# Kernel tuning notes

Measured on AMD Instinct MI355X. Metric: run time of the kernel, lower is better.

The kernel has to match this reference:

```python
import jax, jax.numpy as jnp
import numpy as np

EPS = 1e-7  # tf.keras.backend.epsilon()
ROUTING = 3
C, L = 32, 32

def squash(s):
    # 'Dynamic routing between capsules' squash: (|s|^2/(1+|s|^2)) * s/|s|
    n = jnp.linalg.norm(s, axis=-1, keepdims=True)
    return (n ** 2 / (1 + n ** 2) / (n + EPS)) * s

def setup_inputs() -> dict:
    key = jax.random.key(0)
    k1, k2 = jax.random.split(key)
    B, H, Wd, iC, iL = 32, 8, 8, 32, 32
    inputs = jax.random.normal(k1, (B, H, Wd, iC, iL), dtype=jnp.float32)
    N = H * Wd * iC  # 2048 input capsules
    # glorot_uniform for W: [N, input_L, C*L]
    limit = float(np.sqrt(6.0 / (iL + C * L)))
    W = jax.random.uniform(k2, (N, iL, C * L), minval=-limit, maxval=limit, dtype=jnp.float32)
    biases = jnp.zeros((C, L), dtype=jnp.float32)  # 'zeros' initializer
    return {"inputs": inputs, "W": W, "biases": biases}

def reference(inputs, W, biases):
    B = inputs.shape[0]
    N, iL = W.shape[0], W.shape[1]
    x = inputs.reshape(B, N, iL)
    # per-capsule prediction: u[b,j,k] = sum_i x[b,j,i] * W[j,i,k]
    u = jnp.einsum('bji,jik->bjk', x, W).reshape(B, N, C, L)
    b = jnp.zeros((B, N, C, 1), dtype=u.dtype)
    v = jnp.zeros((B, C, L), dtype=u.dtype)
    for r in range(ROUTING):
        c = jax.nn.softmax(b, axis=2)                 # coupling coeffs over C
        s = jnp.sum(u * c, axis=1) + biases           # [B,C,L]
        # NOTE: CapsuleAttentionBlock applied here in original (source not
        # provided in this module); treated as identity.
        v = squash(s)                                 # [B,C,L]
        if r < ROUTING - 1:
            b = b + jnp.sum(u * v[:, None, :, :], axis=-1, keepdims=True)
    return v
```

## Files before the change

kernel.cpp:

```cpp
#include <hip/hip_runtime.h>
#include <hip/hip_bf16.h>

#define NB    32
#define NCAP  2048
#define CDIM  32
#define LDIM  32
#define ILEN  32
#define CL    1024

__device__ inline unsigned short f32_to_bf16_rne(float f) {
    unsigned int u = __float_as_uint(f);
    unsigned int r = 0x7FFFu + ((u >> 16) & 1u);
    u += r;
    return (unsigned short)(u >> 16);
}
__device__ inline float bf16_to_f32(unsigned short h) {
    return __uint_as_float(((unsigned int)h) << 16);
}

__global__ __launch_bounds__(256) void compute_u(const float* __restrict__ x,
                                                 const float* __restrict__ W,
                                                 unsigned short* __restrict__ u) {
    const int j  = blockIdx.x >> 2;
    const int kq = blockIdx.x & 3;
    const int t  = threadIdx.x;

    __shared__ float wl[32 * 256];
    __shared__ float xs[32 * 32];

    const float* Wj = W + (size_t)j * (ILEN * CL) + kq * 256;
#pragma unroll
    for (int it = 0; it < 8; ++it) {
        int f   = t + it * 256;
        int i   = f >> 6;
        int col = (f & 63) << 2;
        float4 v = *(const float4*)(Wj + (size_t)i * CL + col);
        *(float4*)(wl + i * 256 + col) = v;
    }
    {
        int b = t >> 3;
        int i = (t & 7) << 2;
        float4 v = *(const float4*)(x + (size_t)b * (NCAP * ILEN) + (size_t)j * ILEN + i);
        *(float4*)(xs + b * 32 + i) = v;
    }
    __syncthreads();

    const int lane = t & 63;
    const int wv   = t >> 6;

    float4 acc[8];
#pragma unroll
    for (int bb = 0; bb < 8; ++bb) acc[bb] = make_float4(0.f, 0.f, 0.f, 0.f);

#pragma unroll 4
    for (int i = 0; i < 32; ++i) {
        float4 w4 = *(const float4*)(wl + i * 256 + (lane << 2));
#pragma unroll
        for (int bb = 0; bb < 8; ++bb) {
            float xv = xs[(wv * 8 + bb) * 32 + i];
            acc[bb].x += xv * w4.x;
            acc[bb].y += xv * w4.y;
            acc[bb].z += xv * w4.z;
            acc[bb].w += xv * w4.w;
        }
    }

    const int k = kq * 256 + (lane << 2);
#pragma unroll
    for (int bb = 0; bb < 8; ++bb) {
        int b = wv * 8 + bb;
        ushort4 o;
        o.x = f32_to_bf16_rne(acc[bb].x);
        o.y = f32_to_bf16_rne(acc[bb].y);
        o.z = f32_to_bf16_rne(acc[bb].z);
        o.w = f32_to_bf16_rne(acc[bb].w);
        *(ushort4*)(u + ((size_t)b * NCAP + j) * CL + k) = o;
    }
}

__global__ __launch_bounds__(256) void route_pass(const unsigned short* __restrict__ u,
                                                  const float* __restrict__ vlog,
                                                  float* __restrict__ s_out) {
    const int b  = blockIdx.x;
    const int jc = blockIdx.y;
    const int t  = threadIdx.x;

    __shared__ float vl[1024];
    __shared__ float blog[32];
    __shared__ float cpl[32];

    {
        float4 v = *(const float4*)(vlog + b * 1024 + t * 4);
        *(float4*)(vl + t * 4) = v;
    }
    __syncthreads();

    const int c  = t >> 3;
    const int l4 = (t & 7) << 2;
    const float4 vme = *(const float4*)(vl + c * 32 + l4);

    float4 acc = make_float4(0.f, 0.f, 0.f, 0.f);
    const unsigned short* ub = u + ((size_t)b * NCAP + (size_t)jc * 64) * CL + t * 4;

    ushort4 uu = *(const ushort4*)(ub);
    for (int jj = 0; jj < 64; ++jj) {
        float4 uf;
        uf.x = bf16_to_f32(uu.x);
        uf.y = bf16_to_f32(uu.y);
        uf.z = bf16_to_f32(uu.z);
        uf.w = bf16_to_f32(uu.w);

        ushort4 uu_next;
        if (jj + 1 < 64) uu_next = *(const ushort4*)(ub + (size_t)(jj + 1) * CL);

        float p = uf.x * vme.x + uf.y * vme.y + uf.z * vme.z + uf.w * vme.w;
        p += __shfl_xor(p, 1, 64);
        p += __shfl_xor(p, 2, 64);
        p += __shfl_xor(p, 4, 64);
        if ((t & 7) == 0) blog[c] = p;
        __syncthreads();

        if (t < 64) {
            int ci = t & 31;
            float val = blog[ci];
            float m = val;
            m = fmaxf(m, __shfl_xor(m, 16, 64));
            m = fmaxf(m, __shfl_xor(m, 8, 64));
            m = fmaxf(m, __shfl_xor(m, 4, 64));
            m = fmaxf(m, __shfl_xor(m, 2, 64));
            m = fmaxf(m, __shfl_xor(m, 1, 64));
            float e = __expf(val - m);
            float ssum = e;
            ssum += __shfl_xor(ssum, 16, 64);
            ssum += __shfl_xor(ssum, 8, 64);
            ssum += __shfl_xor(ssum, 4, 64);
            ssum += __shfl_xor(ssum, 2, 64);
            ssum += __shfl_xor(ssum, 1, 64);
            if (t < 32) cpl[ci] = e / ssum;
        }
        __syncthreads();

        float cw = cpl[c];
        acc.x += cw * uf.x;
        acc.y += cw * uf.y;
        acc.z += cw * uf.z;
        acc.w += cw * uf.w;
        uu = uu_next;
    }

    float* sp = s_out + b * 1024 + c * 32 + l4;
    atomicAdd(sp + 0, acc.x);
    atomicAdd(sp + 1, acc.y);
    atomicAdd(sp + 2, acc.z);
    atomicAdd(sp + 3, acc.w);
}

__global__ __launch_bounds__(256) void squash_kernel(const float* __restrict__ s,
                                                     const float* __restrict__ biases,
                                                     float* __restrict__ vout,
                                                     float* __restrict__ vlog_out,
                                                     const float* __restrict__ vprev) {
    const int b = blockIdx.x;
    const int t = threadIdx.x;

    float4 sv = *(const float4*)(s + b * 1024 + t * 4);
    float4 bi = *(const float4*)(biases + t * 4);
    sv.x += bi.x; sv.y += bi.y; sv.z += bi.z; sv.w += bi.w;

    float n2 = sv.x * sv.x + sv.y * sv.y + sv.z * sv.z + sv.w * sv.w;
    n2 += __shfl_xor(n2, 1, 64);
    n2 += __shfl_xor(n2, 2, 64);
    n2 += __shfl_xor(n2, 4, 64);

    float n = sqrtf(n2);
    float f = n2 / (1.f + n2) / (n + 1e-7f);

    float4 v;
    v.x = f * sv.x; v.y = f * sv.y; v.z = f * sv.z; v.w = f * sv.w;
    *(float4*)(vout + b * 1024 + t * 4) = v;

    if (vlog_out != nullptr) {
        float4 a = make_float4(0.f, 0.f, 0.f, 0.f);
        if (vprev != nullptr) a = *(const float4*)(vprev + b * 1024 + t * 4);
        float4 o;
        o.x = v.x + a.x; o.y = v.y + a.y; o.z = v.z + a.z; o.w = v.w + a.w;
        *(float4*)(vlog_out + b * 1024 + t * 4) = o;
    }
}

extern "C" void kernel_launch(void* const* d_in, const int* in_sizes, int n_in,
                              void* d_out, int out_size, void* d_ws, size_t ws_size,
                              hipStream_t stream) {
    const float* x      = (const float*)d_in[0];
    const float* W      = (const float*)d_in[1];
    const float* biases = (const float*)d_in[2];
    float* out = (float*)d_out;

    unsigned short* u = (unsigned short*)d_ws;
    float* fb = (float*)((char*)d_ws + (size_t)NB * NCAP * CL * 2);
    float* s0   = fb + 0 * 32768;
    float* s1   = fb + 1 * 32768;
    float* s2   = fb + 2 * 32768;
    float* zv   = fb + 3 * 32768;
    float* v0   = fb + 4 * 32768;
    float* vl2  = fb + 5 * 32768;
    float* vdmp = fb + 6 * 32768;

    hipMemsetAsync(fb, 0, 4 * 32768 * sizeof(float), stream);

    compute_u<<<NCAP * 4, 256, 0, stream>>>(x, W, u);

    dim3 rg(NB, 32);
    route_pass<<<rg, 256, 0, stream>>>(u, zv, s0);
    squash_kernel<<<NB, 256, 0, stream>>>(s0, biases, v0, nullptr, nullptr);
    route_pass<<<rg, 256, 0, stream>>>(u, v0, s1);
    squash_kernel<<<NB, 256, 0, stream>>>(s1, biases, vdmp, vl2, v0);
    route_pass<<<rg, 256, 0, stream>>>(u, vl2, s2);
    squash_kernel<<<NB, 256, 0, stream>>>(s2, biases, out, nullptr, nullptr);
}
```

Before: 556.6 us.

## Restructure routing pass to per-wave softmax without block barriers and partial sums

The routing kernel is rewritten so each wavefront processes whole input capsules independently. It computes the 32 agreement logits and their softmax with in-wave shuffles, removing the two __syncthreads per capsule and 16-byte bf16 loads. Partial sums are reduced in LDS and written to per-chunk buffers that squash sums, which replaces the atomics and the memset. The first pass skips the softmax and uses a uniform 1/32 coefficient, and compute_u now stores x transposed in LDS to allow vector loads.

```diff
diff --git a/kernel.cpp b/kernel.cpp
--- a/kernel.cpp
+++ b/kernel.cpp
@@ -3,19 +3,24 @@
 
 #define NB    32
 #define NCAP  2048
-#define CDIM  32
-#define LDIM  32
+#define CL    1024
 #define ILEN  32
-#define CL    1024
 
 __device__ inline unsigned short f32_to_bf16_rne(float f) {
     unsigned int u = __float_as_uint(f);
-    unsigned int r = 0x7FFFu + ((u >> 16) & 1u);
-    u += r;
+    u += 0x7FFFu + ((u >> 16) & 1u);
     return (unsigned short)(u >> 16);
 }
-__device__ inline float bf16_to_f32(unsigned short h) {
-    return __uint_as_float(((unsigned int)h) << 16);
+
+__device__ inline void unpack8(uint4 a, float* f) {
+    f[0] = __uint_as_float(a.x << 16);
+    f[1] = __uint_as_float(a.x & 0xFFFF0000u);
+    f[2] = __uint_as_float(a.y << 16);
+    f[3] = __uint_as_float(a.y & 0xFFFF0000u);
+    f[4] = __uint_as_float(a.z << 16);
+    f[5] = __uint_as_float(a.z & 0xFFFF0000u);
+    f[6] = __uint_as_float(a.w << 16);
+    f[7] = __uint_as_float(a.w & 0xFFFF0000u);
 }
 
 __global__ __launch_bounds__(256) void compute_u(const float* __restrict__ x,
@@ -34,34 +39,40 @@
         int f   = t + it * 256;
         int i   = f >> 6;
         int col = (f & 63) << 2;
-        float4 v = *(const float4*)(Wj + (size_t)i * CL + col);
-        *(float4*)(wl + i * 256 + col) = v;
+        *(float4*)(wl + i * 256 + col) = *(const float4*)(Wj + (size_t)i * CL + col);
     }
     {
-        int b = t >> 3;
-        int i = (t & 7) << 2;
-        float4 v = *(const float4*)(x + (size_t)b * (NCAP * ILEN) + (size_t)j * ILEN + i);
-        *(float4*)(xs + b * 32 + i) = v;
+        int b  = t >> 3;
+        int i4 = (t & 7) << 2;
+        float4 v = *(const float4*)(x + ((size_t)b * NCAP + j) * ILEN + i4);
+        xs[(i4 + 0) * 32 + b] = v.x;
+        xs[(i4 + 1) * 32 + b] = v.y;
+        xs[(i4 + 2) * 32 + b] = v.z;
+        xs[(i4 + 3) * 32 + b] = v.w;
     }
     __syncthreads();
 
     const int lane = t & 63;
     const int wv   = t >> 6;
 
-    float4 acc[8];
-#pragma unroll
-    for (int bb = 0; bb < 8; ++bb) acc[bb] = make_float4(0.f, 0.f, 0.f, 0.f);
+    float acc[8][4];
+#pragma unroll
+    for (int bb = 0; bb < 8; ++bb)
+#pragma unroll
+        for (int q = 0; q < 4; ++q) acc[bb][q] = 0.f;
 
 #pragma unroll 4
     for (int i = 0; i < 32; ++i) {
         float4 w4 = *(const float4*)(wl + i * 256 + (lane << 2));
+        float4 xa = *(const float4*)(xs + i * 32 + wv * 8);
+        float4 xb = *(const float4*)(xs + i * 32 + wv * 8 + 4);
+        float xv[8] = {xa.x, xa.y, xa.z, xa.w, xb.x, xb.y, xb.z, xb.w};
 #pragma unroll
         for (int bb = 0; bb < 8; ++bb) {
-            float xv = xs[(wv * 8 + bb) * 32 + i];
-            acc[bb].x += xv * w4.x;
-            acc[bb].y += xv * w4.y;
-            acc[bb].z += xv * w4.z;
-            acc[bb].w += xv * w4.w;
+            acc[bb][0] += xv[bb] * w4.x;
+            acc[bb][1] += xv[bb] * w4.y;
+            acc[bb][2] += xv[bb] * w4.z;
+            acc[bb][3] += xv[bb] * w4.w;
         }
     }
 
@@ -70,92 +81,112 @@
     for (int bb = 0; bb < 8; ++bb) {
         int b = wv * 8 + bb;
         ushort4 o;
-        o.x = f32_to_bf16_rne(acc[bb].x);
-        o.y = f32_to_bf16_rne(acc[bb].y);
-        o.z = f32_to_bf16_rne(acc[bb].z);
-        o.w = f32_to_bf16_rne(acc[bb].w);
+        o.x = f32_to_bf16_rne(acc[bb][0]);
+        o.y = f32_to_bf16_rne(acc[bb][1]);
+        o.z = f32_to_bf16_rne(acc[bb][2]);
+        o.w = f32_to_bf16_rne(acc[bb][3]);
         *(ushort4*)(u + ((size_t)b * NCAP + j) * CL + k) = o;
     }
 }
 
+template<bool HAS_V>
 __global__ __launch_bounds__(256) void route_pass(const unsigned short* __restrict__ u,
                                                   const float* __restrict__ vlog,
-                                                  float* __restrict__ s_out) {
-    const int b  = blockIdx.x;
-    const int jc = blockIdx.y;
-    const int t  = threadIdx.x;
-
-    __shared__ float vl[1024];
-    __shared__ float blog[32];
-    __shared__ float cpl[32];
-
-    {
-        float4 v = *(const float4*)(vlog + b * 1024 + t * 4);
-        *(float4*)(vl + t * 4) = v;
-    }
+                                                  float* __restrict__ spart) {
+    const int b    = blockIdx.x;
+    const int jc   = blockIdx.y;
+    const int t    = threadIdx.x;
+    const int wv   = t >> 6;
+    const int lane = t & 63;
+    const int c0   = lane >> 2;
+    const int sub  = lane & 3;
+    const int e0   = c0 * 32 + sub * 8;
+
+    float vme0[8], vme1[8];
+    if (HAS_V) {
+        const float* vb = vlog + b * CL;
+        *(float4*)(vme0)     = *(const float4*)(vb + e0);
+        *(float4*)(vme0 + 4) = *(const float4*)(vb + e0 + 4);
+        *(float4*)(vme1)     = *(const float4*)(vb + e0 + 512);
+        *(float4*)(vme1 + 4) = *(const float4*)(vb + e0 + 516);
+    }
+
+    const int jbase = jc * 128 + wv * 32;
+    const unsigned short* ub = u + ((size_t)b * NCAP + jbase) * CL;
+
+    float acc0[8], acc1[8];
+#pragma unroll
+    for (int e = 0; e < 8; ++e) { acc0[e] = 0.f; acc1[e] = 0.f; }
+
+    uint4 a0 = *(const uint4*)(ub + 0 * CL + e0);
+    uint4 g0 = *(const uint4*)(ub + 0 * CL + e0 + 512);
+    uint4 a1 = *(const uint4*)(ub + 1 * CL + e0);
+    uint4 g1 = *(const uint4*)(ub + 1 * CL + e0 + 512);
+
+    for (int jj = 0; jj < 32; ++jj) {
+        int jn = (jj + 2 < 32) ? (jj + 2) : 31;
+        uint4 a2 = *(const uint4*)(ub + (size_t)jn * CL + e0);
+        uint4 g2 = *(const uint4*)(ub + (size_t)jn * CL + e0 + 512);
+
+        float uf0[8], uf1[8];
+        unpack8(a0, uf0);
+        unpack8(g0, uf1);
+
+        float cw0, cw1;
+        if (HAS_V) {
+            float p0 = 0.f, p1 = 0.f;
+#pragma unroll
+            for (int e = 0; e < 8; ++e) { p0 += uf0[e] * vme0[e]; p1 += uf1[e] * vme1[e]; }
+            p0 += __shfl_xor(p0, 1); p0 += __shfl_xor(p0, 2);
+            p1 += __shfl_xor(p1, 1); p1 += __shfl_xor(p1, 2);
+            float m = fmaxf(p0, p1);
+            m = fmaxf(m, __shfl_xor(m, 4));
+            m = fmaxf(m, __shfl_xor(m, 8));
+            m = fmaxf(m, __shfl_xor(m, 16));
+            m = fmaxf(m, __shfl_xor(m, 32));
+            float ex0 = __expf(p0 - m);
+            float ex1 = __expf(p1 - m);
+            float ssum = ex0 + ex1;
+            ssum += __shfl_xor(ssum, 4);
+            ssum += __shfl_xor(ssum, 8);
+            ssum += __shfl_xor(ssum, 16);
+            ssum += __shfl_xor(ssum, 32);
+            float inv = __builtin_amdgcn_rcpf(ssum);
+            cw0 = ex0 * inv;
+            cw1 = ex1 * inv;
+        } else {
+            cw0 = 0.03125f;
+            cw1 = 0.03125f;
+        }
+#pragma unroll
+        for (int e = 0; e < 8; ++e) {
+            acc0[e] += cw0 * uf0[e];
+            acc1[e] += cw1 * uf1[e];
+        }
+        a0 = a1; g0 = g1; a1 = a2; g1 = g2;
+    }
+
+    __shared__ float red[4][1024];
+    *(float4*)(&red[wv][e0])       = *(float4*)(acc0);
+    *(float4*)(&red[wv][e0 + 4])   = *(float4*)(acc0 + 4);
+    *(float4*)(&red[wv][e0 + 512]) = *(float4*)(acc1);
+    *(float4*)(&red[wv][e0 + 516]) = *(float4*)(acc1 + 4);
     __syncthreads();
 
-    const int c  = t >> 3;
-    const int l4 = (t & 7) << 2;
-    const float4 vme = *(const float4*)(vl + c * 32 + l4);
-
-    float4 acc = make_float4(0.f, 0.f, 0.f, 0.f);
-    const unsigned short* ub = u + ((size_t)b * NCAP + (size_t)jc * 64) * CL + t * 4;
-
-    ushort4 uu = *(const ushort4*)(ub);
-    for (int jj = 0; jj < 64; ++jj) {
-        float4 uf;
-        uf.x = bf16_to_f32(uu.x);
-        uf.y = bf16_to_f32(uu.y);
-        uf.z = bf16_to_f32(uu.z);
-        uf.w = bf16_to_f32(uu.w);
-
-        ushort4 uu_next;
-        if (jj + 1 < 64) uu_next = *(const ushort4*)(ub + (size_t)(jj + 1) * CL);
-
-        float p = uf.x * vme.x + uf.y * vme.y + uf.z * vme.z + uf.w * vme.w;
-        p += __shfl_xor(p, 1, 64);
-        p += __shfl_xor(p, 2, 64);
-        p += __shfl_xor(p, 4, 64);
-        if ((t & 7) == 0) blog[c] = p;
-        __syncthreads();
-
-        if (t < 64) {
-            int ci = t & 31;
-            float val = blog[ci];
-            float m = val;
-            m = fmaxf(m, __shfl_xor(m, 16, 64));
-            m = fmaxf(m, __shfl_xor(m, 8, 64));
-            m = fmaxf(m, __shfl_xor(m, 4, 64));
-            m = fmaxf(m, __shfl_xor(m, 2, 64));
-            m = fmaxf(m, __shfl_xor(m, 1, 64));
-            float e = __expf(val - m);
-            float ssum = e;
-            ssum += __shfl_xor(ssum, 16, 64);
-            ssum += __shfl_xor(ssum, 8, 64);
-            ssum += __shfl_xor(ssum, 4, 64);
-            ssum += __shfl_xor(ssum, 2, 64);
-            ssum += __shfl_xor(ssum, 1, 64);
-            if (t < 32) cpl[ci] = e / ssum;
-        }
-        __syncthreads();
-
-        float cw = cpl[c];
-        acc.x += cw * uf.x;
-        acc.y += cw * uf.y;
-        acc.z += cw * uf.z;
-        acc.w += cw * uf.w;
-        uu = uu_next;
-    }
-
-    float* sp = s_out + b * 1024 + c * 32 + l4;
-    atomicAdd(sp + 0, acc.x);
-    atomicAdd(sp + 1, acc.y);
-    atomicAdd(sp + 2, acc.z);
-    atomicAdd(sp + 3, acc.w);
-}
-
-__global__ __launch_bounds__(256) void squash_kernel(const float* __restrict__ s,
+    const int o = t * 4;
+    float4 r0 = *(float4*)(&red[0][o]);
+    float4 r1 = *(float4*)(&red[1][o]);
+    float4 r2 = *(float4*)(&red[2][o]);
+    float4 r3 = *(float4*)(&red[3][o]);
+    float4 r;
+    r.x = (r0.x + r1.x) + (r2.x + r3.x);
+    r.y = (r0.y + r1.y) + (r2.y + r3.y);
+    r.z = (r0.z + r1.z) + (r2.z + r3.z);
+    r.w = (r0.w + r1.w) + (r2.w + r3.w);
+    *(float4*)(spart + ((size_t)b * 16 + jc) * CL + o) = r;
+}
+
+__global__ __launch_bounds__(256) void squash_kernel(const float* __restrict__ spart,
                                                      const float* __restrict__ biases,
                                                      float* __restrict__ vout,
                                                      float* __restrict__ vlog_out,
@@ -163,28 +194,33 @@
     const int b = blockIdx.x;
     const int t = threadIdx.x;
 
-    float4 sv = *(const float4*)(s + b * 1024 + t * 4);
+    float4 sv = make_float4(0.f, 0.f, 0.f, 0.f);
+#pragma unroll
+    for (int p = 0; p < 16; ++p) {
+        float4 q = *(const float4*)(spart + ((size_t)b * 16 + p) * CL + t * 4);
+        sv.x += q.x; sv.y += q.y; sv.z += q.z; sv.w += q.w;
+    }
     float4 bi = *(const float4*)(biases + t * 4);
     sv.x += bi.x; sv.y += bi.y; sv.z += bi.z; sv.w += bi.w;
 
     float n2 = sv.x * sv.x + sv.y * sv.y + sv.z * sv.z + sv.w * sv.w;
-    n2 += __shfl_xor(n2, 1, 64);
-    n2 += __shfl_xor(n2, 2, 64);
-    n2 += __shfl_xor(n2, 4, 64);
+    n2 += __shfl_xor(n2, 1);
+    n2 += __shfl_xor(n2, 2);
+    n2 += __shfl_xor(n2, 4);
 
     float n = sqrtf(n2);
-    float f = n2 / (1.f + n2) / (n + 1e-7f);
+    float f = n2 / ((1.f + n2) * (n + 1e-7f));
 
     float4 v;
     v.x = f * sv.x; v.y = f * sv.y; v.z = f * sv.z; v.w = f * sv.w;
-    *(float4*)(vout + b * 1024 + t * 4) = v;
+    *(float4*)(vout + b * CL + t * 4) = v;
 
     if (vlog_out != nullptr) {
         float4 a = make_float4(0.f, 0.f, 0.f, 0.f);
-        if (vprev != nullptr) a = *(const float4*)(vprev + b * 1024 + t * 4);
+        if (vprev != nullptr) a = *(const float4*)(vprev + b * CL + t * 4);
         float4 o;
         o.x = v.x + a.x; o.y = v.y + a.y; o.z = v.z + a.z; o.w = v.w + a.w;
-        *(float4*)(vlog_out + b * 1024 + t * 4) = o;
+        *(float4*)(vlog_out + b * CL + t * 4) = o;
     }
 }
 
@@ -197,24 +233,19 @@
     float* out = (float*)d_out;
 
     unsigned short* u = (unsigned short*)d_ws;
-    float* fb = (float*)((char*)d_ws + (size_t)NB * NCAP * CL * 2);
-    float* s0   = fb + 0 * 32768;
-    float* s1   = fb + 1 * 32768;
-    float* s2   = fb + 2 * 32768;
-    float* zv   = fb + 3 * 32768;
-    float* v0   = fb + 4 * 32768;
-    float* vl2  = fb + 5 * 32768;
-    float* vdmp = fb + 6 * 32768;
-
-    hipMemsetAsync(fb, 0, 4 * 32768 * sizeof(float), stream);
+    float* fb    = (float*)((char*)d_ws + (size_t)NB * NCAP * CL * 2);
+    float* spart = fb;
+    float* v0    = spart + 524288;
+    float* vl2   = v0 + 32768;
+    float* vdmp  = vl2 + 32768;
 
     compute_u<<<NCAP * 4, 256, 0, stream>>>(x, W, u);
 
-    dim3 rg(NB, 32);
-    route_pass<<<rg, 256, 0, stream>>>(u, zv, s0);
-    squash_kernel<<<NB, 256, 0, stream>>>(s0, biases, v0, nullptr, nullptr);
-    route_pass<<<rg, 256, 0, stream>>>(u, v0, s1);
-    squash_kernel<<<NB, 256, 0, stream>>>(s1, biases, vdmp, vl2, v0);
-    route_pass<<<rg, 256, 0, stream>>>(u, vl2, s2);
-    squash_kernel<<<NB, 256, 0, stream>>>(s2, biases, out, nullptr, nullptr);
-}
+    dim3 rg(NB, 16);
+    route_pass<false><<<rg, 256, 0, stream>>>(u, nullptr, spart);
+    squash_kernel<<<NB, 256, 0, stream>>>(spart, biases, v0, nullptr, nullptr);
+    route_pass<true><<<rg, 256, 0, stream>>>(u, v0, spart);
+    squash_kernel<<<NB, 256, 0, stream>>>(spart, biases, vdmp, vl2, v0);
+    route_pass<true><<<rg, 256, 0, stream>>>(u, vl2, spart);
+    squash_kernel<<<NB, 256, 0, stream>>>(spart, biases, out, nullptr, nullptr);
+}
```

After: 461.4 us. 1.21x faster.
